# Kernel optimization log

Measured on AMD Instinct MI355X. Metric: run time of the kernel, lower is better.

The kernel has to match this reference:

```python
import jax, jax.numpy as jnp
import numpy as np

EPS = 1e-7
MIN_NORM = 1e-15
PROJ_EPS = 4e-3
C = 1.0
HEADS = 4
NEG_SLOPE = 0.2

def artanh(x):
    x = jnp.clip(x, -1.0 + EPS, 1.0 - EPS)
    return 0.5 * (jnp.log1p(x) - jnp.log1p(-x))

def _norm(x):
    return jnp.clip(jnp.linalg.norm(x, axis=-1, keepdims=True), MIN_NORM)

def proj(x, c):
    n = _norm(x)
    maxnorm = (1.0 - PROJ_EPS) / jnp.sqrt(c)
    return jnp.where(n > maxnorm, x / n * maxnorm, x)

def expmap0(u, c):
    sc = jnp.sqrt(c)
    n = _norm(u)
    return jnp.tanh(sc * n) * u / (sc * n)

def logmap0(p, c):
    sc = jnp.sqrt(c)
    n = _norm(p)
    return artanh(sc * n) * p / (sc * n)

def mobius_add(x, y, c):
    x2 = jnp.sum(x * x, -1, keepdims=True)
    y2 = jnp.sum(y * y, -1, keepdims=True)
    xy = jnp.sum(x * y, -1, keepdims=True)
    num = (1 + 2 * c * xy + c * y2) * x + (1 - c * x2) * y
    den = 1 + 2 * c * xy + c * c * x2 * y2
    return num / jnp.clip(den, MIN_NORM)

def mobius_matvec(m, x, c):
    sc = jnp.sqrt(c)
    xn = _norm(x)
    mx = x @ m.T
    mxn = _norm(mx)
    res = jnp.tanh(mxn / xn * artanh(sc * xn)) * mx / (mxn * sc)
    zero = jnp.all(mx == 0, axis=-1, keepdims=True)
    return jnp.where(zero, 0.0, res)

def segment_softmax(scores, seg, n):
    # scores: [E, H], seg: [E] destination node ids
    smax = jax.ops.segment_max(scores, seg, num_segments=n)
    smax = jnp.where(jnp.isfinite(smax), smax, 0.0)
    ex = jnp.exp(scores - smax[seg])
    den = jax.ops.segment_sum(ex, seg, num_segments=n)
    return ex / jnp.clip(den[seg], MIN_NORM)


def setup_inputs() -> dict:
    key = jax.random.key(0)
    ks = jax.random.split(key, 6)
    N, D_IN, D_OUT, E = 50000, 128, 128, 800000
    x = 0.01 * jax.random.normal(ks[0], (N, D_IN), dtype=jnp.float32)
    W = (math := np.sqrt(2.0 * 6.0 / (D_IN + D_OUT))) * jax.random.uniform(ks[1], (D_OUT, D_IN), dtype=jnp.float32, minval=-1.0, maxval=1.0)
    lin_bias = jnp.zeros((D_OUT,), jnp.float32)
    att = 0.1 * jax.random.normal(ks[2], (1, HEADS, 2 * (D_OUT // HEADS)), dtype=jnp.float32)
    conv_bias = jnp.zeros((D_OUT,), jnp.float32)
    src = jax.random.randint(ks[3], (E,), 0, N, dtype=jnp.int32)
    # guarantee no self loops (module removes them before adding canonical ones)
    dst = (src + 1 + jax.random.randint(ks[4], (E,), 0, N - 1, dtype=jnp.int32)) % N
    return {"x": x, "W": W, "lin_bias": lin_bias, "att": att,
            "conv_bias": conv_bias, "edge_src": src, "edge_dst": dst}


def reference(x, W, lin_bias, att, conv_bias, edge_src, edge_dst):
    N = x.shape[0]
    H = HEADS
    # ---- HypLinear (c=1, eval mode so no dropout) ----
    h = proj(mobius_matvec(W, x, C), C)
    hyp_bias = proj(expmap0(lin_bias, C), C)   # proj_tan0 is identity on Poincare ball
    h = proj(mobius_add(h, hyp_bias, C), C)
    D = h.shape[-1] // H
    # ---- add self loops ----
    loops = jnp.arange(N, dtype=edge_src.dtype)
    src = jnp.concatenate([edge_src, loops])   # j (source)
    dst = jnp.concatenate([edge_dst, loops])   # i (target / aggregation index)
    # ---- tangent-space GAT message passing ----
    log_x = logmap0(h, C).reshape(N, H, D)
    x_i = log_x[dst]                            # [E, H, D]
    x_j = log_x[src]                            # [E, H, D]
    att_i, att_j = att[0, :, :D], att[0, :, D:]
    alpha = jnp.einsum('ehd,hd->eh', x_i, att_i) + jnp.einsum('ehd,hd->eh', x_j, att_j)
    alpha = jax.nn.leaky_relu(alpha, NEG_SLOPE)
    alpha = segment_softmax(alpha, dst, N)      # [E, H]
    msg = x_j * alpha[:, :, None]
    out = jax.ops.segment_sum(msg, dst, num_segments=N)  # [N, H, D]
    out = out.reshape(N, H * D) + conv_bias
    # ---- update / activation / map back to manifold ----
    out = jax.nn.relu(out)                      # proj_tan0 is identity
    return proj(expmap0(out, C), C)
```

## Files before the change

### kernel.cpp

```cpp
#include <hip/hip_runtime.h>
#include <math.h>

#define EPSF 1e-7f
#define MIN_NORM 1e-15f
#define MAXNORM 0.996f
#define NEG_SLOPE 0.2f

typedef __attribute__((ext_vector_type(8))) short short8;
typedef __attribute__((ext_vector_type(4))) float f32x4;

__device__ __forceinline__ float wave_reduce_sum(float v) {
    #pragma unroll
    for (int m = 1; m < 64; m <<= 1) v += __shfl_xor(v, m, 64);
    return v;
}

__device__ __forceinline__ float artanhf_(float x) {
    x = fminf(fmaxf(x, -1.f + EPSF), 1.f - EPSF);
    return 0.5f * (log1pf(x) - log1pf(-x));
}

__device__ __forceinline__ float lrelu(float a) {
    return a < 0.f ? a * NEG_SLOPE : a;
}

__device__ __forceinline__ unsigned short f2bf(float f) {
    unsigned u = __float_as_uint(f);
    u += 0x7FFFu + ((u >> 16) & 1u);
    return (unsigned short)(u >> 16);
}
__device__ __forceinline__ float bf2f(unsigned short h) {
    return __uint_as_float(((unsigned)h) << 16);
}

__global__ void prep_kernel(const float* __restrict__ W,
                            unsigned short* __restrict__ whi,
                            unsigned short* __restrict__ wlo,
                            const float* __restrict__ lin_bias,
                            float* __restrict__ bbuf) {
    if (blockIdx.x == 64) {
        if (threadIdx.x >= 64) return;
        int lane = threadIdx.x;
        float u0 = lin_bias[lane], u1 = lin_bias[lane + 64];
        float n2 = wave_reduce_sum(u0 * u0 + u1 * u1);
        float n = fmaxf(sqrtf(n2), MIN_NORM);
        float s = tanhf(n) / n;
        float b0 = s * u0, b1 = s * u1;
        float bn = fmaxf(tanhf(n), MIN_NORM);
        float fn2 = bn * bn;
        if (bn > MAXNORM) { float f = MAXNORM / bn; b0 *= f; b1 *= f; fn2 = MAXNORM * MAXNORM; }
        bbuf[lane] = b0;
        bbuf[lane + 64] = b1;
        if (lane == 0) bbuf[128] = fn2;
        return;
    }
    int idx = blockIdx.x * 256 + threadIdx.x;
    int i = idx & 7, l = (idx >> 3) & 63, ts = idx >> 9;
    int s = ts & 3, t = ts >> 2;
    int o = t * 16 + (l & 15);
    int k = s * 32 + ((l >> 4) * 8) + i;
    float f = W[o * 128 + k];
    unsigned short h = f2bf(f);
    unsigned short lo = f2bf(f - bf2f(h));
    whi[idx] = h;
    wlo[idx] = lo;
}

#define DPAD 132
__global__ __launch_bounds__(256) void node_kernel(
    const float* __restrict__ x,
    const unsigned short* __restrict__ whi, const unsigned short* __restrict__ wlo,
    const float* __restrict__ bbuf, const float* __restrict__ att,
    unsigned short* __restrict__ log_xb,
    float* __restrict__ s_i, float* __restrict__ s_j, int N)
{
    __shared__ float mxs[16][DPAD];
    __shared__ float xn2s[16];
    int tid = threadIdx.x, wave = tid >> 6, lane = tid & 63;
    int nbase = blockIdx.x * 16;
    int arow = lane & 15, kgrp = lane >> 4;
    int anode = min(nbase + arow, N - 1);

    f32x4 acc0 = {0.f, 0.f, 0.f, 0.f};
    f32x4 acc1 = {0.f, 0.f, 0.f, 0.f};
    int t0 = wave * 2, t1 = wave * 2 + 1;
    float x2loc = 0.f;

    #pragma unroll
    for (int s = 0; s < 4; ++s) {
        const float* xp = x + (size_t)anode * 128 + s * 32 + kgrp * 8;
        float4 xa = *(const float4*)xp;
        float4 xb = *(const float4*)(xp + 4);
        float xv[8] = {xa.x, xa.y, xa.z, xa.w, xb.x, xb.y, xb.z, xb.w};
        short8 ahi, alo;
        #pragma unroll
        for (int i = 0; i < 8; ++i) {
            unsigned short h = f2bf(xv[i]);
            unsigned short l = f2bf(xv[i] - bf2f(h));
            ahi[i] = (short)h;
            alo[i] = (short)l;
        }
        if (wave == 0) {
            #pragma unroll
            for (int i = 0; i < 8; ++i) x2loc = fmaf(xv[i], xv[i], x2loc);
        }
        short8 bh0 = *(const short8*)(whi + ((size_t)(t0 * 4 + s) * 64 + lane) * 8);
        short8 bl0 = *(const short8*)(wlo + ((size_t)(t0 * 4 + s) * 64 + lane) * 8);
        short8 bh1 = *(const short8*)(whi + ((size_t)(t1 * 4 + s) * 64 + lane) * 8);
        short8 bl1 = *(const short8*)(wlo + ((size_t)(t1 * 4 + s) * 64 + lane) * 8);
        acc0 = __builtin_amdgcn_mfma_f32_16x16x32_bf16(ahi, bh0, acc0, 0, 0, 0);
        acc0 = __builtin_amdgcn_mfma_f32_16x16x32_bf16(alo, bh0, acc0, 0, 0, 0);
        acc0 = __builtin_amdgcn_mfma_f32_16x16x32_bf16(ahi, bl0, acc0, 0, 0, 0);
        acc1 = __builtin_amdgcn_mfma_f32_16x16x32_bf16(ahi, bh1, acc1, 0, 0, 0);
        acc1 = __builtin_amdgcn_mfma_f32_16x16x32_bf16(alo, bh1, acc1, 0, 0, 0);
        acc1 = __builtin_amdgcn_mfma_f32_16x16x32_bf16(ahi, bl1, acc1, 0, 0, 0);
    }
    if (wave == 0) {
        x2loc += __shfl_xor(x2loc, 16, 64);
        x2loc += __shfl_xor(x2loc, 32, 64);
        if (lane < 16) xn2s[lane] = x2loc;
    }
    #pragma unroll
    for (int r = 0; r < 4; ++r) {
        mxs[kgrp * 4 + r][t0 * 16 + arow] = acc0[r];
        mxs[kgrp * 4 + r][t1 * 16 + arow] = acc1[r];
    }
    __syncthreads();

    int g16 = lane >> 4, l16 = lane & 15;
    int nn = wave * 4 + g16;
    int node = nbase + nn;
    if (node < N) {
        int head = l16 >> 2;
        int dbase = l16 * 8;
        int dd8 = (l16 & 3) * 8;
        float bb[8], aiv[8], ajv[8];
        #pragma unroll
        for (int j = 0; j < 8; ++j) {
            bb[j] = bbuf[dbase + j];
            aiv[j] = att[head * 64 + dd8 + j];
            ajv[j] = att[head * 64 + 32 + dd8 + j];
        }
        float y2 = bbuf[128];

        float4 va = *(const float4*)&mxs[nn][dbase];
        float4 vb = *(const float4*)&mxs[nn][dbase + 4];
        float v[8] = {va.x, va.y, va.z, va.w, vb.x, vb.y, vb.z, vb.w};

        float mq = 0.f;
        #pragma unroll
        for (int j = 0; j < 8; ++j) mq = fmaf(v[j], v[j], mq);
        #pragma unroll
        for (int m = 1; m < 16; m <<= 1) mq += __shfl_xor(mq, m, 64);

        float xn2 = xn2s[nn];
        float xn = fmaxf(sqrtf(xn2), MIN_NORM);
        float mxn = fmaxf(sqrtf(mq), MIN_NORM);
        float t = tanhf(mxn / xn * artanhf_(xn));
        float scl = t / mxn;
        bool zero = (mq == 0.f);
        float r[8];
        #pragma unroll
        for (int j = 0; j < 8; ++j) r[j] = zero ? 0.f : scl * v[j];
        float rn2 = zero ? 0.f : t * t;
        float rn = zero ? MIN_NORM : fmaxf(fabsf(t), MIN_NORM);
        float x2 = rn2;
        if (rn > MAXNORM) {
            float f = MAXNORM / rn;
            #pragma unroll
            for (int j = 0; j < 8; ++j) r[j] *= f;
            x2 = MAXNORM * MAXNORM;
        }
        float xy = 0.f;
        #pragma unroll
        for (int j = 0; j < 8; ++j) xy = fmaf(r[j], bb[j], xy);
        #pragma unroll
        for (int m = 1; m < 16; m <<= 1) xy += __shfl_xor(xy, m, 64);
        float cA = 1.f + 2.f * xy + y2;
        float cB = 1.f - x2;
        float dn = fmaxf(1.f + 2.f * xy + x2 * y2, MIN_NORM);
        float inv = 1.f / dn;
        float h[8];
        #pragma unroll
        for (int j = 0; j < 8; ++j) h[j] = (cA * r[j] + cB * bb[j]) * inv;
        float hq = 0.f;
        #pragma unroll
        for (int j = 0; j < 8; ++j) hq = fmaf(h[j], h[j], hq);
        #pragma unroll
        for (int m = 1; m < 16; m <<= 1) hq += __shfl_xor(hq, m, 64);
        float hn = fmaxf(sqrtf(hq), MIN_NORM);
        float ln2 = hq;
        if (hn > MAXNORM) {
            float f = MAXNORM / hn;
            #pragma unroll
            for (int j = 0; j < 8; ++j) h[j] *= f;
            ln2 = MAXNORM * MAXNORM;
        }
        float lnn = fmaxf(sqrtf(ln2), MIN_NORM);
        float ls = artanhf_(lnn) / lnn;
        float lv[8];
        #pragma unroll
        for (int j = 0; j < 8; ++j) lv[j] = ls * h[j];
        uint4 pk;
        pk.x = (unsigned)f2bf(lv[0]) | ((unsigned)f2bf(lv[1]) << 16);
        pk.y = (unsigned)f2bf(lv[2]) | ((unsigned)f2bf(lv[3]) << 16);
        pk.z = (unsigned)f2bf(lv[4]) | ((unsigned)f2bf(lv[5]) << 16);
        pk.w = (unsigned)f2bf(lv[6]) | ((unsigned)f2bf(lv[7]) << 16);
        *(uint4*)&log_xb[(size_t)node * 128 + dbase] = pk;
        float pi = 0.f, pj = 0.f;
        #pragma unroll
        for (int j = 0; j < 8; ++j) {
            pi = fmaf(lv[j], aiv[j], pi);
            pj = fmaf(lv[j], ajv[j], pj);
        }
        pi += __shfl_xor(pi, 1, 64); pi += __shfl_xor(pi, 2, 64);
        pj += __shfl_xor(pj, 1, 64); pj += __shfl_xor(pj, 2, 64);
        if ((l16 & 3) == 0) {
            s_i[(size_t)node * 4 + head] = pi;
            s_j[(size_t)node * 4 + head] = pj;
        }
    }
}

__global__ void build_kernel(const int* __restrict__ src, const int* __restrict__ dst,
                             int E, int* __restrict__ head, int2* __restrict__ pair)
{
    int e = blockIdx.x * blockDim.x + threadIdx.x;
    if (e >= E) return;
    int s_ = src[e], d_ = dst[e];
    int prev = atomicExch(&head[(size_t)d_ * 16 + (e & 15)], e);
    pair[e] = make_int2(s_, prev);
}

#define MAXS 128
__global__ __launch_bounds__(256) void aggregate_kernel(
    const int* __restrict__ head, const int2* __restrict__ pair,
    const float* __restrict__ s_i, const float* __restrict__ s_j,
    const unsigned short* __restrict__ log_xb, const float* __restrict__ conv_bias,
    float* __restrict__ out, int N)
{
    __shared__ __align__(16) int slist[4][MAXS];
    __shared__ int scnt[4];
    int tid = threadIdx.x, wave = tid >> 6, lane = tid & 63;
    int n = blockIdx.x * 4 + wave;
    bool valid = n < N;

    if (lane == 0) scnt[wave] = 0;
    __syncthreads();

    int resume = -1;
    if (valid && lane < 16) {
        int e = head[(size_t)n * 16 + lane];
        while (e >= 0) {
            int2 pr = pair[e];
            int pos = atomicAdd(&scnt[wave], 1);
            if (pos < MAXS) {
                slist[wave][pos] = pr.x;
                e = pr.y;
            } else { resume = e; break; }
        }
    }
    __syncthreads();

    int g = lane >> 5;
    float acc0 = 0.f, acc1 = 0.f, dna = 0.f, dnb = 0.f;
    float sia = 0.f, sib = 0.f;

#define EDGE_PROC(sid) do { \
    float aa_ = s_j[(size_t)(sid) * 4 + g], ab_ = s_j[(size_t)(sid) * 4 + 2 + g]; \
    float eA_ = __expf(lrelu(sia + aa_)), eB_ = __expf(lrelu(sib + ab_)); \
    dna += eA_; dnb += eB_; \
    acc0 = fmaf(eA_, bf2f(log_xb[(size_t)(sid) * 128 + lane]), acc0); \
    acc1 = fmaf(eB_, bf2f(log_xb[(size_t)(sid) * 128 + 64 + lane]), acc1); \
} while (0)

    int deg = 0;
    if (valid) {
        deg = min(scnt[wave], MAXS);
        float4 si = *(const float4*)(s_i + (size_t)n * 4);
        float4 sjn = *(const float4*)(s_j + (size_t)n * 4);
        sia = g == 0 ? si.x : si.y; sib = g == 0 ? si.z : si.w;
        float sjna = g == 0 ? sjn.x : sjn.y, sjnb = g == 0 ? sjn.z : sjn.w;

        float ea = __expf(lrelu(sia + sjna));
        float eb = __expf(lrelu(sib + sjnb));
        dna = ea; dnb = eb;
        acc0 = ea * bf2f(log_xb[(size_t)n * 128 + lane]);
        acc1 = eb * bf2f(log_xb[(size_t)n * 128 + 64 + lane]);

        const int* sl = slist[wave];
        int i = 0;
        for (; i + 4 <= deg; i += 4) {
            int4 sq = *(const int4*)&sl[i];
            int s0 = sq.x, s1 = sq.y, s2 = sq.z, s3 = sq.w;
            float a0a = s_j[(size_t)s0 * 4 + g],     a0b = s_j[(size_t)s0 * 4 + 2 + g];
            float a1a = s_j[(size_t)s1 * 4 + g],     a1b = s_j[(size_t)s1 * 4 + 2 + g];
            float a2a = s_j[(size_t)s2 * 4 + g],     a2b = s_j[(size_t)s2 * 4 + 2 + g];
            float a3a = s_j[(size_t)s3 * 4 + g],     a3b = s_j[(size_t)s3 * 4 + 2 + g];
            unsigned short m0a = log_xb[(size_t)s0 * 128 + lane], m0b = log_xb[(size_t)s0 * 128 + 64 + lane];
            unsigned short m1a = log_xb[(size_t)s1 * 128 + lane], m1b = log_xb[(size_t)s1 * 128 + 64 + lane];
            unsigned short m2a = log_xb[(size_t)s2 * 128 + lane], m2b = log_xb[(size_t)s2 * 128 + 64 + lane];
            unsigned short m3a = log_xb[(size_t)s3 * 128 + lane], m3b = log_xb[(size_t)s3 * 128 + 64 + lane];
            float e0a = __expf(lrelu(sia + a0a)), e0b = __expf(lrelu(sib + a0b));
            float e1a = __expf(lrelu(sia + a1a)), e1b = __expf(lrelu(sib + a1b));
            float e2a = __expf(lrelu(sia + a2a)), e2b = __expf(lrelu(sib + a2b));
            float e3a = __expf(lrelu(sia + a3a)), e3b = __expf(lrelu(sib + a3b));
            dna += e0a + e1a + e2a + e3a;
            dnb += e0b + e1b + e2b + e3b;
            acc0 = fmaf(e0a, bf2f(m0a), acc0);
            acc1 = fmaf(e0b, bf2f(m0b), acc1);
            acc0 = fmaf(e1a, bf2f(m1a), acc0);
            acc1 = fmaf(e1b, bf2f(m1b), acc1);
            acc0 = fmaf(e2a, bf2f(m2a), acc0);
            acc1 = fmaf(e2b, bf2f(m2b), acc1);
            acc0 = fmaf(e3a, bf2f(m3a), acc0);
            acc1 = fmaf(e3b, bf2f(m3b), acc1);
        }
        for (; i < deg; ++i) {
            int s_ = sl[i];
            EDGE_PROC(s_);
        }
    }

    unsigned long long mask = __ballot(resume >= 0);
    while (mask) {
        int l = __ffsll((long long)mask) - 1;
        int e = __shfl(resume, l, 64);
        while (e >= 0) {
            int sv = 0, nx = -1;
            if (lane == 0) { int2 pr = pair[e]; sv = pr.x; nx = pr.y; }
            sv = __shfl(sv, 0, 64);
            e = __shfl(nx, 0, 64);
            EDGE_PROC(sv);
        }
        mask &= mask - 1;
    }
#undef EDGE_PROC

    if (!valid) return;

    float v0 = acc0 / fmaxf(dna, MIN_NORM) + conv_bias[lane];
    float v1 = acc1 / fmaxf(dnb, MIN_NORM) + conv_bias[lane + 64];
    v0 = fmaxf(v0, 0.f);
    v1 = fmaxf(v1, 0.f);
    float n2 = wave_reduce_sum(v0 * v0 + v1 * v1);
    float nn = fmaxf(sqrtf(n2), MIN_NORM);
    float tv = tanhf(nn);
    float s = tv / nn;
    float r0 = s * v0, r1 = s * v1;
    float rn = fmaxf(tv, MIN_NORM);
    if (rn > MAXNORM) { float f = MAXNORM / rn; r0 *= f; r1 *= f; }
    out[(size_t)n * 128 + lane] = r0;
    out[(size_t)n * 128 + 64 + lane] = r1;
}

extern "C" void kernel_launch(void* const* d_in, const int* in_sizes, int n_in,
                              void* d_out, int out_size, void* d_ws, size_t ws_size,
                              hipStream_t stream)
{
    const float* x        = (const float*)d_in[0];
    const float* W        = (const float*)d_in[1];
    const float* lin_bias = (const float*)d_in[2];
    const float* att      = (const float*)d_in[3];
    const float* conv_bias= (const float*)d_in[4];
    const int*   esrc     = (const int*)d_in[5];
    const int*   edst     = (const int*)d_in[6];
    int N = in_sizes[0] / 128;
    int E = in_sizes[5];
    float* out = (float*)d_out;

    char* p = (char*)d_ws;
    float* bbuf   = (float*)p;  p += 256 * 4;
    unsigned short* whi = (unsigned short*)p; p += 16384 * 2;
    unsigned short* wlo = (unsigned short*)p; p += 16384 * 2;
    float* s_i    = (float*)p;  p += (size_t)N * 4 * 4;
    float* s_j    = (float*)p;  p += (size_t)N * 4 * 4;
    int*   head   = (int*)p;    p += (size_t)N * 16 * 4;
    int2*  pair   = (int2*)p;   p += (size_t)E * 8;
    unsigned short* log_xb = (unsigned short*)p; p += (size_t)N * 128 * 2;

    hipMemsetAsync(head, 0xFF, (size_t)N * 16 * 4, stream);

    prep_kernel<<<65, 256, 0, stream>>>(W, whi, wlo, lin_bias, bbuf);
    build_kernel<<<(E + 255) / 256, 256, 0, stream>>>(esrc, edst, E, head, pair);
    int nTiles = (N + 15) / 16;
    node_kernel<<<nTiles, 256, 0, stream>>>(x, whi, wlo, bbuf, att, log_xb, s_i, s_j, N);
    aggregate_kernel<<<(N + 3) / 4, 256, 0, stream>>>(
        head, pair, s_i, s_j, log_xb, conv_bias, out, N);
}
```

Baseline: 134.6 us.

## Interleave bf16 log features per lane and unroll aggregation gather by eight

```diff
diff --git a/kernel.cpp b/kernel.cpp
--- a/kernel.cpp
+++ b/kernel.cpp
@@ -71,7 +71,7 @@
     const float* __restrict__ x,
     const unsigned short* __restrict__ whi, const unsigned short* __restrict__ wlo,
     const float* __restrict__ bbuf, const float* __restrict__ att,
-    unsigned short* __restrict__ log_xb,
+    unsigned* __restrict__ logp,
     float* __restrict__ s_i, float* __restrict__ s_j, int N)
 {
     __shared__ float mxs[16][DPAD];
@@ -130,95 +130,111 @@
     int g16 = lane >> 4, l16 = lane & 15;
     int nn = wave * 4 + g16;
     int node = nbase + nn;
-    if (node < N) {
-        int head = l16 >> 2;
-        int dbase = l16 * 8;
-        int dd8 = (l16 & 3) * 8;
-        float bb[8], aiv[8], ajv[8];
+    bool valid = node < N;
+    int head = l16 >> 2;
+    int dbase = l16 * 8;
+    int dd8 = (l16 & 3) * 8;
+    float bb[8], aiv[8], ajv[8];
+    #pragma unroll
+    for (int j = 0; j < 8; ++j) {
+        bb[j] = bbuf[dbase + j];
+        aiv[j] = att[head * 64 + dd8 + j];
+        ajv[j] = att[head * 64 + 32 + dd8 + j];
+    }
+    float y2 = bbuf[128];
+
+    float4 va = *(const float4*)&mxs[nn][dbase];
+    float4 vb = *(const float4*)&mxs[nn][dbase + 4];
+    float v[8] = {va.x, va.y, va.z, va.w, vb.x, vb.y, vb.z, vb.w};
+
+    float mq = 0.f;
+    #pragma unroll
+    for (int j = 0; j < 8; ++j) mq = fmaf(v[j], v[j], mq);
+    #pragma unroll
+    for (int m = 1; m < 16; m <<= 1) mq += __shfl_xor(mq, m, 64);
+
+    float xn2 = xn2s[nn];
+    float xn = fmaxf(sqrtf(xn2), MIN_NORM);
+    float mxn = fmaxf(sqrtf(mq), MIN_NORM);
+    float t = tanhf(mxn / xn * artanhf_(xn));
+    float scl = t / mxn;
+    bool zero = (mq == 0.f);
+    float r[8];
+    #pragma unroll
+    for (int j = 0; j < 8; ++j) r[j] = zero ? 0.f : scl * v[j];
+    float rn2 = zero ? 0.f : t * t;
+    float rn = zero ? MIN_NORM : fmaxf(fabsf(t), MIN_NORM);
+    float x2 = rn2;
+    if (rn > MAXNORM) {
+        float f = MAXNORM / rn;
         #pragma unroll
-        for (int j = 0; j < 8; ++j) {
-            bb[j] = bbuf[dbase + j];
-            aiv[j] = att[head * 64 + dd8 + j];
-            ajv[j] = att[head * 64 + 32 + dd8 + j];
-        }
-        float y2 = bbuf[128];
-
-        float4 va = *(const float4*)&mxs[nn][dbase];
-        float4 vb = *(const float4*)&mxs[nn][dbase + 4];
-        float v[8] = {va.x, va.y, va.z, va.w, vb.x, vb.y, vb.z, vb.w};
-
-        float mq = 0.f;
+        for (int j = 0; j < 8; ++j) r[j] *= f;
+        x2 = MAXNORM * MAXNORM;
+    }
+    float xy = 0.f;
+    #pragma unroll
+    for (int j = 0; j < 8; ++j) xy = fmaf(r[j], bb[j], xy);
+    #pragma unroll
+    for (int m = 1; m < 16; m <<= 1) xy += __shfl_xor(xy, m, 64);
+    float cA = 1.f + 2.f * xy + y2;
+    float cB = 1.f - x2;
+    float dn = fmaxf(1.f + 2.f * xy + x2 * y2, MIN_NORM);
+    float inv = 1.f / dn;
+    float h[8];
+    #pragma unroll
+    for (int j = 0; j < 8; ++j) h[j] = (cA * r[j] + cB * bb[j]) * inv;
+    float hq = 0.f;
+    #pragma unroll
+    for (int j = 0; j < 8; ++j) hq = fmaf(h[j], h[j], hq);
+    #pragma unroll
+    for (int m = 1; m < 16; m <<= 1) hq += __shfl_xor(hq, m, 64);
+    float hn = fmaxf(sqrtf(hq), MIN_NORM);
+    float ln2 = hq;
+    if (hn > MAXNORM) {
+        float f = MAXNORM / hn;
         #pragma unroll
-        for (int j = 0; j < 8; ++j) mq = fmaf(v[j], v[j], mq);
-        #pragma unroll
-        for (int m = 1; m < 16; m <<= 1) mq += __shfl_xor(mq, m, 64);
-
-        float xn2 = xn2s[nn];
-        float xn = fmaxf(sqrtf(xn2), MIN_NORM);
-        float mxn = fmaxf(sqrtf(mq), MIN_NORM);
-        float t = tanhf(mxn / xn * artanhf_(xn));
-        float scl = t / mxn;
-        bool zero = (mq == 0.f);
-        float r[8];
-        #pragma unroll
-        for (int j = 0; j < 8; ++j) r[j] = zero ? 0.f : scl * v[j];
-        float rn2 = zero ? 0.f : t * t;
-        float rn = zero ? MIN_NORM : fmaxf(fabsf(t), MIN_NORM);
-        float x2 = rn2;
-        if (rn > MAXNORM) {
-            float f = MAXNORM / rn;
-            #pragma unroll
-            for (int j = 0; j < 8; ++j) r[j] *= f;
-            x2 = MAXNORM * MAXNORM;
-        }
-        float xy = 0.f;
-        #pragma unroll
-        for (int j = 0; j < 8; ++j) xy = fmaf(r[j], bb[j], xy);
-        #pragma unroll
-        for (int m = 1; m < 16; m <<= 1) xy += __shfl_xor(xy, m, 64);
-        float cA = 1.f + 2.f * xy + y2;
-        float cB = 1.f - x2;
-        float dn = fmaxf(1.f + 2.f * xy + x2 * y2, MIN_NORM);
-        float inv = 1.f / dn;
-        float h[8];
-        #pragma unroll
-        for (int j = 0; j < 8; ++j) h[j] = (cA * r[j] + cB * bb[j]) * inv;
-        float hq = 0.f;
-        #pragma unroll
-        for (int j = 0; j < 8; ++j) hq = fmaf(h[j], h[j], hq);
-        #pragma unroll
-        for (int m = 1; m < 16; m <<= 1) hq += __shfl_xor(hq, m, 64);
-        float hn = fmaxf(sqrtf(hq), MIN_NORM);
-        float ln2 = hq;
-        if (hn > MAXNORM) {
-            float f = MAXNORM / hn;
-            #pragma unroll
-            for (int j = 0; j < 8; ++j) h[j] *= f;
-            ln2 = MAXNORM * MAXNORM;
-        }
-        float lnn = fmaxf(sqrtf(ln2), MIN_NORM);
-        float ls = artanhf_(lnn) / lnn;
-        float lv[8];
-        #pragma unroll
-        for (int j = 0; j < 8; ++j) lv[j] = ls * h[j];
-        uint4 pk;
-        pk.x = (unsigned)f2bf(lv[0]) | ((unsigned)f2bf(lv[1]) << 16);
-        pk.y = (unsigned)f2bf(lv[2]) | ((unsigned)f2bf(lv[3]) << 16);
-        pk.z = (unsigned)f2bf(lv[4]) | ((unsigned)f2bf(lv[5]) << 16);
-        pk.w = (unsigned)f2bf(lv[6]) | ((unsigned)f2bf(lv[7]) << 16);
-        *(uint4*)&log_xb[(size_t)node * 128 + dbase] = pk;
-        float pi = 0.f, pj = 0.f;
-        #pragma unroll
-        for (int j = 0; j < 8; ++j) {
-            pi = fmaf(lv[j], aiv[j], pi);
-            pj = fmaf(lv[j], ajv[j], pj);
-        }
-        pi += __shfl_xor(pi, 1, 64); pi += __shfl_xor(pi, 2, 64);
-        pj += __shfl_xor(pj, 1, 64); pj += __shfl_xor(pj, 2, 64);
-        if ((l16 & 3) == 0) {
-            s_i[(size_t)node * 4 + head] = pi;
-            s_j[(size_t)node * 4 + head] = pj;
-        }
+        for (int j = 0; j < 8; ++j) h[j] *= f;
+        ln2 = MAXNORM * MAXNORM;
+    }
+    float lnn = fmaxf(sqrtf(ln2), MIN_NORM);
+    float ls = artanhf_(lnn) / lnn;
+    float lv[8];
+    #pragma unroll
+    for (int j = 0; j < 8; ++j) lv[j] = ls * h[j];
+
+    unsigned o0 = (unsigned)f2bf(lv[0]) | ((unsigned)f2bf(lv[1]) << 16);
+    unsigned o1 = (unsigned)f2bf(lv[2]) | ((unsigned)f2bf(lv[3]) << 16);
+    unsigned o2 = (unsigned)f2bf(lv[4]) | ((unsigned)f2bf(lv[5]) << 16);
+    unsigned o3 = (unsigned)f2bf(lv[6]) | ((unsigned)f2bf(lv[7]) << 16);
+    unsigned p0 = __shfl_xor(o0, 8, 64);
+    unsigned p1 = __shfl_xor(o1, 8, 64);
+    unsigned p2 = __shfl_xor(o2, 8, 64);
+    unsigned p3 = __shfl_xor(o3, 8, 64);
+    if (valid && l16 < 8) {
+        uint4 q0, q1;
+        q0.x = (o0 & 0xffffu) | (p0 << 16);
+        q0.y = (o0 >> 16)     | (p0 & 0xffff0000u);
+        q0.z = (o1 & 0xffffu) | (p1 << 16);
+        q0.w = (o1 >> 16)     | (p1 & 0xffff0000u);
+        q1.x = (o2 & 0xffffu) | (p2 << 16);
+        q1.y = (o2 >> 16)     | (p2 & 0xffff0000u);
+        q1.z = (o3 & 0xffffu) | (p3 << 16);
+        q1.w = (o3 >> 16)     | (p3 & 0xffff0000u);
+        *(uint4*)&logp[(size_t)node * 64 + l16 * 8] = q0;
+        *(uint4*)&logp[(size_t)node * 64 + l16 * 8 + 4] = q1;
+    }
+    float pi = 0.f, pj = 0.f;
+    #pragma unroll
+    for (int j = 0; j < 8; ++j) {
+        pi = fmaf(lv[j], aiv[j], pi);
+        pj = fmaf(lv[j], ajv[j], pj);
+    }
+    pi += __shfl_xor(pi, 1, 64); pi += __shfl_xor(pi, 2, 64);
+    pj += __shfl_xor(pj, 1, 64); pj += __shfl_xor(pj, 2, 64);
+    if (valid && (l16 & 3) == 0) {
+        int pos = ((head & 1) << 1) | (head >> 1);
+        s_i[(size_t)node * 4 + pos] = pi;
+        s_j[(size_t)node * 4 + pos] = pj;
     }
 }
 
@@ -236,7 +252,7 @@
 __global__ __launch_bounds__(256) void aggregate_kernel(
     const int* __restrict__ head, const int2* __restrict__ pair,
     const float* __restrict__ s_i, const float* __restrict__ s_j,
-    const unsigned short* __restrict__ log_xb, const float* __restrict__ conv_bias,
+    const unsigned* __restrict__ logp, const float* __restrict__ conv_bias,
     float* __restrict__ out, int N)
 {
     __shared__ __align__(16) int slist[4][MAXS];
@@ -267,54 +283,49 @@
     float sia = 0.f, sib = 0.f;
 
 #define EDGE_PROC(sid) do { \
-    float aa_ = s_j[(size_t)(sid) * 4 + g], ab_ = s_j[(size_t)(sid) * 4 + 2 + g]; \
-    float eA_ = __expf(lrelu(sia + aa_)), eB_ = __expf(lrelu(sib + ab_)); \
+    float2 sj_ = *(const float2*)(s_j + (size_t)(sid) * 4 + g * 2); \
+    unsigned pk_ = logp[(size_t)(sid) * 64 + lane]; \
+    float eA_ = __expf(lrelu(sia + sj_.x)), eB_ = __expf(lrelu(sib + sj_.y)); \
     dna += eA_; dnb += eB_; \
-    acc0 = fmaf(eA_, bf2f(log_xb[(size_t)(sid) * 128 + lane]), acc0); \
-    acc1 = fmaf(eB_, bf2f(log_xb[(size_t)(sid) * 128 + 64 + lane]), acc1); \
+    acc0 = fmaf(eA_, bf2f((unsigned short)(pk_ & 0xffffu)), acc0); \
+    acc1 = fmaf(eB_, bf2f((unsigned short)(pk_ >> 16)), acc1); \
 } while (0)
 
     int deg = 0;
     if (valid) {
         deg = min(scnt[wave], MAXS);
-        float4 si = *(const float4*)(s_i + (size_t)n * 4);
-        float4 sjn = *(const float4*)(s_j + (size_t)n * 4);
-        sia = g == 0 ? si.x : si.y; sib = g == 0 ? si.z : si.w;
-        float sjna = g == 0 ? sjn.x : sjn.y, sjnb = g == 0 ? sjn.z : sjn.w;
-
-        float ea = __expf(lrelu(sia + sjna));
-        float eb = __expf(lrelu(sib + sjnb));
+        float2 si2  = *(const float2*)(s_i + (size_t)n * 4 + g * 2);
+        float2 sj2n = *(const float2*)(s_j + (size_t)n * 4 + g * 2);
+        sia = si2.x; sib = si2.y;
+
+        float ea = __expf(lrelu(sia + sj2n.x));
+        float eb = __expf(lrelu(sib + sj2n.y));
         dna = ea; dnb = eb;
-        acc0 = ea * bf2f(log_xb[(size_t)n * 128 + lane]);
-        acc1 = eb * bf2f(log_xb[(size_t)n * 128 + 64 + lane]);
+        unsigned pks = logp[(size_t)n * 64 + lane];
+        acc0 = ea * bf2f((unsigned short)(pks & 0xffffu));
+        acc1 = eb * bf2f((unsigned short)(pks >> 16));
 
         const int* sl = slist[wave];
         int i = 0;
-        for (; i + 4 <= deg; i += 4) {
-            int4 sq = *(const int4*)&sl[i];
-            int s0 = sq.x, s1 = sq.y, s2 = sq.z, s3 = sq.w;
-            float a0a = s_j[(size_t)s0 * 4 + g],     a0b = s_j[(size_t)s0 * 4 + 2 + g];
-            float a1a = s_j[(size_t)s1 * 4 + g],     a1b = s_j[(size_t)s1 * 4 + 2 + g];
-            float a2a = s_j[(size_t)s2 * 4 + g],     a2b = s_j[(size_t)s2 * 4 + 2 + g];
-            float a3a = s_j[(size_t)s3 * 4 + g],     a3b = s_j[(size_t)s3 * 4 + 2 + g];
-            unsigned short m0a = log_xb[(size_t)s0 * 128 + lane], m0b = log_xb[(size_t)s0 * 128 + 64 + lane];
-            unsigned short m1a = log_xb[(size_t)s1 * 128 + lane], m1b = log_xb[(size_t)s1 * 128 + 64 + lane];
-            unsigned short m2a = log_xb[(size_t)s2 * 128 + lane], m2b = log_xb[(size_t)s2 * 128 + 64 + lane];
-            unsigned short m3a = log_xb[(size_t)s3 * 128 + lane], m3b = log_xb[(size_t)s3 * 128 + 64 + lane];
-            float e0a = __expf(lrelu(sia + a0a)), e0b = __expf(lrelu(sib + a0b));
-            float e1a = __expf(lrelu(sia + a1a)), e1b = __expf(lrelu(sib + a1b));
-            float e2a = __expf(lrelu(sia + a2a)), e2b = __expf(lrelu(sib + a2b));
-            float e3a = __expf(lrelu(sia + a3a)), e3b = __expf(lrelu(sib + a3b));
-            dna += e0a + e1a + e2a + e3a;
-            dnb += e0b + e1b + e2b + e3b;
-            acc0 = fmaf(e0a, bf2f(m0a), acc0);
-            acc1 = fmaf(e0b, bf2f(m0b), acc1);
-            acc0 = fmaf(e1a, bf2f(m1a), acc0);
-            acc1 = fmaf(e1b, bf2f(m1b), acc1);
-            acc0 = fmaf(e2a, bf2f(m2a), acc0);
-            acc1 = fmaf(e2b, bf2f(m2b), acc1);
-            acc0 = fmaf(e3a, bf2f(m3a), acc0);
-            acc1 = fmaf(e3b, bf2f(m3b), acc1);
+        for (; i + 8 <= deg; i += 8) {
+            int4 sqa = *(const int4*)&sl[i];
+            int4 sqb = *(const int4*)&sl[i + 4];
+            int ss[8] = {sqa.x, sqa.y, sqa.z, sqa.w, sqb.x, sqb.y, sqb.z, sqb.w};
+            float2 sj[8];
+            unsigned pk[8];
+            #pragma unroll
+            for (int j = 0; j < 8; ++j) {
+                sj[j] = *(const float2*)(s_j + (size_t)ss[j] * 4 + g * 2);
+                pk[j] = logp[(size_t)ss[j] * 64 + lane];
+            }
+            #pragma unroll
+            for (int j = 0; j < 8; ++j) {
+                float eA = __expf(lrelu(sia + sj[j].x));
+                float eB = __expf(lrelu(sib + sj[j].y));
+                dna += eA; dnb += eB;
+                acc0 = fmaf(eA, bf2f((unsigned short)(pk[j] & 0xffffu)), acc0);
+                acc1 = fmaf(eB, bf2f((unsigned short)(pk[j] >> 16)), acc1);
+            }
         }
         for (; i < deg; ++i) {
             int s_ = sl[i];
@@ -377,14 +388,14 @@
     float* s_j    = (float*)p;  p += (size_t)N * 4 * 4;
     int*   head   = (int*)p;    p += (size_t)N * 16 * 4;
     int2*  pair   = (int2*)p;   p += (size_t)E * 8;
-    unsigned short* log_xb = (unsigned short*)p; p += (size_t)N * 128 * 2;
+    unsigned* logp = (unsigned*)p; p += (size_t)N * 64 * 4;
 
     hipMemsetAsync(head, 0xFF, (size_t)N * 16 * 4, stream);
 
     prep_kernel<<<65, 256, 0, stream>>>(W, whi, wlo, lin_bias, bbuf);
     build_kernel<<<(E + 255) / 256, 256, 0, stream>>>(esrc, edst, E, head, pair);
     int nTiles = (N + 15) / 16;
-    node_kernel<<<nTiles, 256, 0, stream>>>(x, whi, wlo, bbuf, att, log_xb, s_i, s_j, N);
+    node_kernel<<<nTiles, 256, 0, stream>>>(x, whi, wlo, bbuf, att, logp, s_i, s_j, N);
     aggregate_kernel<<<(N + 3) / 4, 256, 0, stream>>>(
-        head, pair, s_i, s_j, log_xb, conv_bias, out, N);
-}
+        head, pair, s_i, s_j, logp, conv_bias, out, N);
+}
```

After: 138.9 us. +3.2%, slower.

## Precompute per-edge fp16 attention weights in edge build kernel

Applied to the files above, without the earlier changes.

```diff
diff --git a/kernel.cpp b/kernel.cpp
--- a/kernel.cpp
+++ b/kernel.cpp
@@ -1,4 +1,5 @@
 #include <hip/hip_runtime.h>
+#include <hip/hip_fp16.h>
 #include <math.h>
 
 #define EPSF 1e-7f
@@ -130,116 +131,135 @@
     int g16 = lane >> 4, l16 = lane & 15;
     int nn = wave * 4 + g16;
     int node = nbase + nn;
-    if (node < N) {
-        int head = l16 >> 2;
-        int dbase = l16 * 8;
-        int dd8 = (l16 & 3) * 8;
-        float bb[8], aiv[8], ajv[8];
+    bool valid = node < N;
+    int head = l16 >> 2;
+    int dbase = l16 * 8;
+    int dd8 = (l16 & 3) * 8;
+    float bb[8], aiv[8], ajv[8];
+    #pragma unroll
+    for (int j = 0; j < 8; ++j) {
+        bb[j] = bbuf[dbase + j];
+        aiv[j] = att[head * 64 + dd8 + j];
+        ajv[j] = att[head * 64 + 32 + dd8 + j];
+    }
+    float y2 = bbuf[128];
+
+    float4 va = *(const float4*)&mxs[nn][dbase];
+    float4 vb = *(const float4*)&mxs[nn][dbase + 4];
+    float v[8] = {va.x, va.y, va.z, va.w, vb.x, vb.y, vb.z, vb.w};
+
+    float mq = 0.f;
+    #pragma unroll
+    for (int j = 0; j < 8; ++j) mq = fmaf(v[j], v[j], mq);
+    #pragma unroll
+    for (int m = 1; m < 16; m <<= 1) mq += __shfl_xor(mq, m, 64);
+
+    float xn2 = xn2s[nn];
+    float xn = fmaxf(sqrtf(xn2), MIN_NORM);
+    float mxn = fmaxf(sqrtf(mq), MIN_NORM);
+    float t = tanhf(mxn / xn * artanhf_(xn));
+    float scl = t / mxn;
+    bool zero = (mq == 0.f);
+    float r[8];
+    #pragma unroll
+    for (int j = 0; j < 8; ++j) r[j] = zero ? 0.f : scl * v[j];
+    float rn2 = zero ? 0.f : t * t;
+    float rn = zero ? MIN_NORM : fmaxf(fabsf(t), MIN_NORM);
+    float x2 = rn2;
+    if (rn > MAXNORM) {
+        float f = MAXNORM / rn;
         #pragma unroll
-        for (int j = 0; j < 8; ++j) {
-            bb[j] = bbuf[dbase + j];
-            aiv[j] = att[head * 64 + dd8 + j];
-            ajv[j] = att[head * 64 + 32 + dd8 + j];
-        }
-        float y2 = bbuf[128];
-
-        float4 va = *(const float4*)&mxs[nn][dbase];
-        float4 vb = *(const float4*)&mxs[nn][dbase + 4];
-        float v[8] = {va.x, va.y, va.z, va.w, vb.x, vb.y, vb.z, vb.w};
-
-        float mq = 0.f;
+        for (int j = 0; j < 8; ++j) r[j] *= f;
+        x2 = MAXNORM * MAXNORM;
+    }
+    float xy = 0.f;
+    #pragma unroll
+    for (int j = 0; j < 8; ++j) xy = fmaf(r[j], bb[j], xy);
+    #pragma unroll
+    for (int m = 1; m < 16; m <<= 1) xy += __shfl_xor(xy, m, 64);
+    float cA = 1.f + 2.f * xy + y2;
+    float cB = 1.f - x2;
+    float dn = fmaxf(1.f + 2.f * xy + x2 * y2, MIN_NORM);
+    float inv = 1.f / dn;
+    float h[8];
+    #pragma unroll
+    for (int j = 0; j < 8; ++j) h[j] = (cA * r[j] + cB * bb[j]) * inv;
+    float hq = 0.f;
+    #pragma unroll
+    for (int j = 0; j < 8; ++j) hq = fmaf(h[j], h[j], hq);
+    #pragma unroll
+    for (int m = 1; m < 16; m <<= 1) hq += __shfl_xor(hq, m, 64);
+    float hn = fmaxf(sqrtf(hq), MIN_NORM);
+    float ln2 = hq;
+    if (hn > MAXNORM) {
+        float f = MAXNORM / hn;
         #pragma unroll
-        for (int j = 0; j < 8; ++j) mq = fmaf(v[j], v[j], mq);
-        #pragma unroll
-        for (int m = 1; m < 16; m <<= 1) mq += __shfl_xor(mq, m, 64);
-
-        float xn2 = xn2s[nn];
-        float xn = fmaxf(sqrtf(xn2), MIN_NORM);
-        float mxn = fmaxf(sqrtf(mq), MIN_NORM);
-        float t = tanhf(mxn / xn * artanhf_(xn));
-        float scl = t / mxn;
-        bool zero = (mq == 0.f);
-        float r[8];
-        #pragma unroll
-        for (int j = 0; j < 8; ++j) r[j] = zero ? 0.f : scl * v[j];
-        float rn2 = zero ? 0.f : t * t;
-        float rn = zero ? MIN_NORM : fmaxf(fabsf(t), MIN_NORM);
-        float x2 = rn2;
-        if (rn > MAXNORM) {
-            float f = MAXNORM / rn;
-            #pragma unroll
-            for (int j = 0; j < 8; ++j) r[j] *= f;
-            x2 = MAXNORM * MAXNORM;
-        }
-        float xy = 0.f;
-        #pragma unroll
-        for (int j = 0; j < 8; ++j) xy = fmaf(r[j], bb[j], xy);
-        #pragma unroll
-        for (int m = 1; m < 16; m <<= 1) xy += __shfl_xor(xy, m, 64);
-        float cA = 1.f + 2.f * xy + y2;
-        float cB = 1.f - x2;
-        float dn = fmaxf(1.f + 2.f * xy + x2 * y2, MIN_NORM);
-        float inv = 1.f / dn;
-        float h[8];
-        #pragma unroll
-        for (int j = 0; j < 8; ++j) h[j] = (cA * r[j] + cB * bb[j]) * inv;
-        float hq = 0.f;
-        #pragma unroll
-        for (int j = 0; j < 8; ++j) hq = fmaf(h[j], h[j], hq);
-        #pragma unroll
-        for (int m = 1; m < 16; m <<= 1) hq += __shfl_xor(hq, m, 64);
-        float hn = fmaxf(sqrtf(hq), MIN_NORM);
-        float ln2 = hq;
-        if (hn > MAXNORM) {
-            float f = MAXNORM / hn;
-            #pragma unroll
-            for (int j = 0; j < 8; ++j) h[j] *= f;
-            ln2 = MAXNORM * MAXNORM;
-        }
-        float lnn = fmaxf(sqrtf(ln2), MIN_NORM);
-        float ls = artanhf_(lnn) / lnn;
-        float lv[8];
-        #pragma unroll
-        for (int j = 0; j < 8; ++j) lv[j] = ls * h[j];
+        for (int j = 0; j < 8; ++j) h[j] *= f;
+        ln2 = MAXNORM * MAXNORM;
+    }
+    float lnn = fmaxf(sqrtf(ln2), MIN_NORM);
+    float ls = artanhf_(lnn) / lnn;
+    float lv[8];
+    #pragma unroll
+    for (int j = 0; j < 8; ++j) lv[j] = ls * h[j];
+
+    if (valid) {
         uint4 pk;
         pk.x = (unsigned)f2bf(lv[0]) | ((unsigned)f2bf(lv[1]) << 16);
         pk.y = (unsigned)f2bf(lv[2]) | ((unsigned)f2bf(lv[3]) << 16);
         pk.z = (unsigned)f2bf(lv[4]) | ((unsigned)f2bf(lv[5]) << 16);
         pk.w = (unsigned)f2bf(lv[6]) | ((unsigned)f2bf(lv[7]) << 16);
         *(uint4*)&log_xb[(size_t)node * 128 + dbase] = pk;
-        float pi = 0.f, pj = 0.f;
-        #pragma unroll
-        for (int j = 0; j < 8; ++j) {
-            pi = fmaf(lv[j], aiv[j], pi);
-            pj = fmaf(lv[j], ajv[j], pj);
-        }
-        pi += __shfl_xor(pi, 1, 64); pi += __shfl_xor(pi, 2, 64);
-        pj += __shfl_xor(pj, 1, 64); pj += __shfl_xor(pj, 2, 64);
-        if ((l16 & 3) == 0) {
-            s_i[(size_t)node * 4 + head] = pi;
-            s_j[(size_t)node * 4 + head] = pj;
-        }
-    }
-}
-
-__global__ void build_kernel(const int* __restrict__ src, const int* __restrict__ dst,
-                             int E, int* __restrict__ head, int2* __restrict__ pair)
+    }
+    float pi = 0.f, pj = 0.f;
+    #pragma unroll
+    for (int j = 0; j < 8; ++j) {
+        pi = fmaf(lv[j], aiv[j], pi);
+        pj = fmaf(lv[j], ajv[j], pj);
+    }
+    pi += __shfl_xor(pi, 1, 64); pi += __shfl_xor(pi, 2, 64);
+    pj += __shfl_xor(pj, 1, 64); pj += __shfl_xor(pj, 2, 64);
+    if (valid && (l16 & 3) == 0) {
+        int pos = ((head & 1) << 1) | (head >> 1);
+        s_i[(size_t)node * 4 + pos] = pi;
+        s_j[(size_t)node * 4 + pos] = pj;
+    }
+}
+
+__global__ void buildw_kernel(const int* __restrict__ src, const int* __restrict__ dst,
+                              int E, const float* __restrict__ s_i,
+                              const float* __restrict__ s_j,
+                              int* __restrict__ head, int4* __restrict__ pair16)
 {
     int e = blockIdx.x * blockDim.x + threadIdx.x;
     if (e >= E) return;
     int s_ = src[e], d_ = dst[e];
     int prev = atomicExch(&head[(size_t)d_ * 16 + (e & 15)], e);
-    pair[e] = make_int2(s_, prev);
+    float4 si = *(const float4*)(s_i + (size_t)d_ * 4);
+    float4 sj = *(const float4*)(s_j + (size_t)s_ * 4);
+    float w0 = __expf(lrelu(si.x + sj.x));
+    float w1 = __expf(lrelu(si.y + sj.y));
+    float w2 = __expf(lrelu(si.z + sj.z));
+    float w3 = __expf(lrelu(si.w + sj.w));
+    __half2 h01 = __floats2half2_rn(w0, w1);
+    __half2 h23 = __floats2half2_rn(w2, w3);
+    int4 pr;
+    pr.x = s_ << 8;
+    pr.y = prev;
+    pr.z = *(int*)&h01;
+    pr.w = *(int*)&h23;
+    pair16[e] = pr;
 }
 
 #define MAXS 128
 __global__ __launch_bounds__(256) void aggregate_kernel(
-    const int* __restrict__ head, const int2* __restrict__ pair,
+    const int* __restrict__ head, const int4* __restrict__ pair16,
     const float* __restrict__ s_i, const float* __restrict__ s_j,
     const unsigned short* __restrict__ log_xb, const float* __restrict__ conv_bias,
     float* __restrict__ out, int N)
 {
     __shared__ __align__(16) int slist[4][MAXS];
+    __shared__ __align__(16) unsigned wlist[4][MAXS * 2];
     __shared__ int scnt[4];
     int tid = threadIdx.x, wave = tid >> 6, lane = tid & 63;
     int n = blockIdx.x * 4 + wave;
@@ -252,10 +272,12 @@
     if (valid && lane < 16) {
         int e = head[(size_t)n * 16 + lane];
         while (e >= 0) {
-            int2 pr = pair[e];
+            int4 pr = pair16[e];
             int pos = atomicAdd(&scnt[wave], 1);
             if (pos < MAXS) {
                 slist[wave][pos] = pr.x;
+                wlist[wave][pos * 2]     = (unsigned)pr.z;
+                wlist[wave][pos * 2 + 1] = (unsigned)pr.w;
                 e = pr.y;
             } else { resume = e; break; }
         }
@@ -264,61 +286,51 @@
 
     int g = lane >> 5;
     float acc0 = 0.f, acc1 = 0.f, dna = 0.f, dnb = 0.f;
-    float sia = 0.f, sib = 0.f;
-
-#define EDGE_PROC(sid) do { \
-    float aa_ = s_j[(size_t)(sid) * 4 + g], ab_ = s_j[(size_t)(sid) * 4 + 2 + g]; \
-    float eA_ = __expf(lrelu(sia + aa_)), eB_ = __expf(lrelu(sib + ab_)); \
-    dna += eA_; dnb += eB_; \
-    acc0 = fmaf(eA_, bf2f(log_xb[(size_t)(sid) * 128 + lane]), acc0); \
-    acc1 = fmaf(eB_, bf2f(log_xb[(size_t)(sid) * 128 + 64 + lane]), acc1); \
-} while (0)
 
     int deg = 0;
     if (valid) {
         deg = min(scnt[wave], MAXS);
-        float4 si = *(const float4*)(s_i + (size_t)n * 4);
-        float4 sjn = *(const float4*)(s_j + (size_t)n * 4);
-        sia = g == 0 ? si.x : si.y; sib = g == 0 ? si.z : si.w;
-        float sjna = g == 0 ? sjn.x : sjn.y, sjnb = g == 0 ? sjn.z : sjn.w;
-
-        float ea = __expf(lrelu(sia + sjna));
-        float eb = __expf(lrelu(sib + sjnb));
+        float2 si2  = *(const float2*)(s_i + (size_t)n * 4 + g * 2);
+        float2 sj2n = *(const float2*)(s_j + (size_t)n * 4 + g * 2);
+        float ea = __expf(lrelu(si2.x + sj2n.x));
+        float eb = __expf(lrelu(si2.y + sj2n.y));
         dna = ea; dnb = eb;
-        acc0 = ea * bf2f(log_xb[(size_t)n * 128 + lane]);
-        acc1 = eb * bf2f(log_xb[(size_t)n * 128 + 64 + lane]);
+        const unsigned short* mrow = log_xb + (size_t)n * 128;
+        acc0 = ea * bf2f(mrow[lane]);
+        acc1 = eb * bf2f(mrow[lane + 64]);
 
         const int* sl = slist[wave];
+        const unsigned* wlv = wlist[wave];
         int i = 0;
         for (; i + 4 <= deg; i += 4) {
-            int4 sq = *(const int4*)&sl[i];
-            int s0 = sq.x, s1 = sq.y, s2 = sq.z, s3 = sq.w;
-            float a0a = s_j[(size_t)s0 * 4 + g],     a0b = s_j[(size_t)s0 * 4 + 2 + g];
-            float a1a = s_j[(size_t)s1 * 4 + g],     a1b = s_j[(size_t)s1 * 4 + 2 + g];
-            float a2a = s_j[(size_t)s2 * 4 + g],     a2b = s_j[(size_t)s2 * 4 + 2 + g];
-            float a3a = s_j[(size_t)s3 * 4 + g],     a3b = s_j[(size_t)s3 * 4 + 2 + g];
-            unsigned short m0a = log_xb[(size_t)s0 * 128 + lane], m0b = log_xb[(size_t)s0 * 128 + 64 + lane];
-            unsigned short m1a = log_xb[(size_t)s1 * 128 + lane], m1b = log_xb[(size_t)s1 * 128 + 64 + lane];
-            unsigned short m2a = log_xb[(size_t)s2 * 128 + lane], m2b = log_xb[(size_t)s2 * 128 + 64 + lane];
-            unsigned short m3a = log_xb[(size_t)s3 * 128 + lane], m3b = log_xb[(size_t)s3 * 128 + 64 + lane];
-            float e0a = __expf(lrelu(sia + a0a)), e0b = __expf(lrelu(sib + a0b));
-            float e1a = __expf(lrelu(sia + a1a)), e1b = __expf(lrelu(sib + a1b));
-            float e2a = __expf(lrelu(sia + a2a)), e2b = __expf(lrelu(sib + a2b));
-            float e3a = __expf(lrelu(sia + a3a)), e3b = __expf(lrelu(sib + a3b));
-            dna += e0a + e1a + e2a + e3a;
-            dnb += e0b + e1b + e2b + e3b;
-            acc0 = fmaf(e0a, bf2f(m0a), acc0);
-            acc1 = fmaf(e0b, bf2f(m0b), acc1);
-            acc0 = fmaf(e1a, bf2f(m1a), acc0);
-            acc1 = fmaf(e1b, bf2f(m1b), acc1);
-            acc0 = fmaf(e2a, bf2f(m2a), acc0);
-            acc1 = fmaf(e2b, bf2f(m2b), acc1);
-            acc0 = fmaf(e3a, bf2f(m3a), acc0);
-            acc1 = fmaf(e3b, bf2f(m3b), acc1);
+            int4 offq = *(const int4*)&sl[i];
+            int offs[4] = {offq.x, offq.y, offq.z, offq.w};
+            unsigned ww[4];
+            unsigned short ma[4], mb[4];
+            #pragma unroll
+            for (int j = 0; j < 4; ++j) {
+                ww[j] = wlv[(i + j) * 2 + g];
+                const unsigned short* mr =
+                    (const unsigned short*)((const char*)log_xb + offs[j]);
+                ma[j] = mr[lane];
+                mb[j] = mr[lane + 64];
+            }
+            #pragma unroll
+            for (int j = 0; j < 4; ++j) {
+                float2 wf = __half22float2(*(const __half2*)&ww[j]);
+                dna += wf.x; dnb += wf.y;
+                acc0 = fmaf(wf.x, bf2f(ma[j]), acc0);
+                acc1 = fmaf(wf.y, bf2f(mb[j]), acc1);
+            }
         }
         for (; i < deg; ++i) {
-            int s_ = sl[i];
-            EDGE_PROC(s_);
+            unsigned w = wlv[i * 2 + g];
+            const unsigned short* mr =
+                (const unsigned short*)((const char*)log_xb + sl[i]);
+            float2 wf = __half22float2(*(const __half2*)&w);
+            dna += wf.x; dnb += wf.y;
+            acc0 = fmaf(wf.x, bf2f(mr[lane]), acc0);
+            acc1 = fmaf(wf.y, bf2f(mr[lane + 64]), acc1);
         }
     }
 
@@ -327,15 +339,21 @@
         int l = __ffsll((long long)mask) - 1;
         int e = __shfl(resume, l, 64);
         while (e >= 0) {
-            int sv = 0, nx = -1;
-            if (lane == 0) { int2 pr = pair[e]; sv = pr.x; nx = pr.y; }
-            sv = __shfl(sv, 0, 64);
+            int off = 0, nx = -1, wz = 0, wwd = 0;
+            if (lane == 0) { int4 pr = pair16[e]; off = pr.x; nx = pr.y; wz = pr.z; wwd = pr.w; }
+            off = __shfl(off, 0, 64);
+            wz = __shfl(wz, 0, 64);
+            wwd = __shfl(wwd, 0, 64);
             e = __shfl(nx, 0, 64);
-            EDGE_PROC(sv);
+            unsigned wsel = (unsigned)(g ? wwd : wz);
+            float2 wf = __half22float2(*(const __half2*)&wsel);
+            const unsigned short* mr = (const unsigned short*)((const char*)log_xb + off);
+            dna += wf.x; dnb += wf.y;
+            acc0 = fmaf(wf.x, bf2f(mr[lane]), acc0);
+            acc1 = fmaf(wf.y, bf2f(mr[lane + 64]), acc1);
         }
         mask &= mask - 1;
     }
-#undef EDGE_PROC
 
     if (!valid) return;
 
@@ -376,15 +394,15 @@
     float* s_i    = (float*)p;  p += (size_t)N * 4 * 4;
     float* s_j    = (float*)p;  p += (size_t)N * 4 * 4;
     int*   head   = (int*)p;    p += (size_t)N * 16 * 4;
-    int2*  pair   = (int2*)p;   p += (size_t)E * 8;
+    int4*  pair16 = (int4*)p;   p += (size_t)E * 16;
     unsigned short* log_xb = (unsigned short*)p; p += (size_t)N * 128 * 2;
 
     hipMemsetAsync(head, 0xFF, (size_t)N * 16 * 4, stream);
 
     prep_kernel<<<65, 256, 0, stream>>>(W, whi, wlo, lin_bias, bbuf);
-    build_kernel<<<(E + 255) / 256, 256, 0, stream>>>(esrc, edst, E, head, pair);
     int nTiles = (N + 15) / 16;
     node_kernel<<<nTiles, 256, 0, stream>>>(x, whi, wlo, bbuf, att, log_xb, s_i, s_j, N);
+    buildw_kernel<<<(E + 255) / 256, 256, 0, stream>>>(esrc, edst, E, s_i, s_j, head, pair16);
     aggregate_kernel<<<(N + 3) / 4, 256, 0, stream>>>(
-        head, pair, s_i, s_j, log_xb, conv_bias, out, N);
-}
+        head, pair16, s_i, s_j, log_xb, conv_bias, out, N);
+}
```

New measurement: 130.3 us. 1.03x faster.
